# Kernel tuning notes

Hardware: AMD Instinct MI355X
Metric: run time of the kernel (lower is better)

Reference implementation:

```python
import jax, jax.numpy as jnp
import numpy as np
import math

D_MODEL = 1024
NUM_HEADS = 16
D_K = D_MODEL // NUM_HEADS
THETA = 10000.0
B, T = 2, 2048


def _trunc_normal(key, shape, std):
    # truncated normal in [-3std, 3std]
    return jax.random.truncated_normal(key, -3.0, 3.0, shape, jnp.float32) * std


def setup_inputs() -> dict:
    key = jax.random.key(0)
    ks = jax.random.split(key, 6)
    sigma = math.sqrt(2.0 / (D_MODEL + D_MODEL))
    x = jax.random.normal(ks[0], (B, T, D_MODEL), jnp.float32)
    Wq = _trunc_normal(ks[1], (D_MODEL, D_MODEL), sigma)  # [out, in]
    Wk = _trunc_normal(ks[2], (D_MODEL, D_MODEL), sigma)
    Wv = _trunc_normal(ks[3], (D_MODEL, D_MODEL), sigma)
    Wo = _trunc_normal(ks[4], (D_MODEL, D_MODEL), sigma)
    token_positions = jnp.arange(T, dtype=jnp.int64 if jax.config.read('jax_enable_x64') else jnp.int32)
    return {"x": x, "Wq": Wq, "Wk": Wk, "Wv": Wv, "Wo": Wo,
            "token_positions": token_positions}


def _rotate_half(x):
    x0 = x[..., ::2]
    x1 = x[..., 1::2]
    return jnp.stack((-x1, x0), axis=-1).reshape(x.shape)


def _rope(x, token_positions):
    # x: [B, H, T, d_k]; token_positions: [T]
    inv_freq = 1.0 / (THETA ** (jnp.arange(0, D_K, 2, dtype=jnp.float32) / D_K))
    ang = token_positions.astype(jnp.float32)[:, None] * inv_freq  # [T, d_k/2]
    cos = jnp.repeat(jnp.cos(ang), 2, axis=-1)  # [T, d_k]
    sin = jnp.repeat(jnp.sin(ang), 2, axis=-1)
    xdtype = x.dtype
    xf = x.astype(jnp.float32)
    return (xf * cos + _rotate_half(xf) * sin).astype(xdtype)


def reference(x, Wq, Wk, Wv, Wo, token_positions):
    b, t, _ = x.shape

    def proj_split(W):
        h = jnp.einsum('btd,od->bto', x, W)
        return h.reshape(b, t, NUM_HEADS, D_K).transpose(0, 2, 1, 3)  # [B,H,T,d_k]

    Q = _rope(proj_split(Wq), token_positions)
    K = _rope(proj_split(Wk), token_positions)
    V = proj_split(Wv)

    scores = jnp.einsum('bhqd,bhkd->bhqk', Q, K) / math.sqrt(D_K)
    causal = jnp.tril(jnp.ones((t, t), dtype=bool))  # [T,T]
    scores = jnp.where(causal, scores, -jnp.inf)
    weights = jax.nn.softmax(scores, axis=-1)
    attn = jnp.einsum('bhqk,bhkd->bhqd', weights, V)  # [B,H,T,d_v]
    merged = attn.transpose(0, 2, 1, 3).reshape(b, t, D_MODEL)
    return jnp.einsum('btd,od->bto', merged, Wo)
```

## Files before the change

### kernel.cpp

```cpp
#include <hip/hip_runtime.h>
#include <cstdint>
#include <cstddef>

#define DMODEL 1024
#define NHEADS 16
#define DKH    64
#define SEQT   2048
#define NBATCH 2
#define MTOT   (NBATCH*SEQT)

#define QSCALE 0.1803368801111204f

using h16   = _Float16;
using h16x2 = __attribute__((ext_vector_type(2))) h16;
using h16x4 = __attribute__((ext_vector_type(4))) h16;
using h16x8 = __attribute__((ext_vector_type(8))) h16;
using f32x4 = __attribute__((ext_vector_type(4))) float;
using fp16x2_native = __attribute__((ext_vector_type(2))) __fp16;

using as1_void = __attribute__((address_space(1))) void;
using as3_void = __attribute__((address_space(3))) void;

__device__ __forceinline__ void gll16(void* lds, const void* g) {
  __builtin_amdgcn_global_load_lds((const as1_void*)g, (as3_void*)lds, 16, 0, 0);
}

__device__ __forceinline__ h16x2 pkrtz(float a, float b) {
  fp16x2_native t = __builtin_amdgcn_cvt_pkrtz(a, b);
  h16x2 r; r[0] = (h16)t[0]; r[1] = (h16)t[1]; return r;
}

__device__ __forceinline__ h16x4 cvt4(const float4 v) {
  h16x4 o; o[0] = (h16)v.x; o[1] = (h16)v.y; o[2] = (h16)v.z; o[3] = (h16)v.w; return o;
}

__global__ void prep_kernel(const float4* __restrict__ x,
                            const float4* __restrict__ Wq, const float4* __restrict__ Wk,
                            const float4* __restrict__ Wv, const float4* __restrict__ Wo,
                            h16x4* __restrict__ xb,
                            h16x4* __restrict__ wqb, h16x4* __restrict__ wkb,
                            h16x4* __restrict__ wvb, h16x4* __restrict__ wob,
                            float* __restrict__ ctab, float* __restrict__ stab) {
  const int tid  = blockIdx.x * blockDim.x + threadIdx.x;
  const int nthr = gridDim.x * blockDim.x;
  const int NX4 = MTOT * DMODEL / 4;
  const int NW4 = DMODEL * DMODEL / 4;
  for (int i = tid; i < NX4; i += nthr) xb[i] = cvt4(x[i]);
  for (int i = tid; i < NW4; i += nthr) {
    wqb[i] = cvt4(Wq[i]);
    wkb[i] = cvt4(Wk[i]);
    wvb[i] = cvt4(Wv[i]);
    wob[i] = cvt4(Wo[i]);
  }
  for (int i = tid; i < SEQT * 32; i += nthr) {
    const int t = i >> 5, fi = i & 31;
    float inv = __expf(-0.28782313662425575f * (float)fi);
    float ang = (float)t * inv;
    float s, c;
    sincosf(ang, &s, &c);
    ctab[i] = c; stab[i] = s;
  }
}

__device__ __forceinline__ void gemm128_bt(const h16* __restrict__ A, const h16* __restrict__ Bt,
                                           int m0, int n0, h16* Al, h16* Bl, f32x4 acc[4][4]) {
  const int tid  = threadIdx.x;
  const int lane = tid & 63;
  const int wv   = tid >> 6;
  const int wm = (wv >> 1) * 64, wn = (wv & 1) * 64;
  const int lr = lane & 15, lk = (lane >> 4) * 8;
  const int srow = tid >> 2, scol = (tid & 3) * 8;
  const h16* a0 = A  + (size_t)(m0 + srow) * DMODEL + scol;
  const h16* a1 = a0 + (size_t)64 * DMODEL;
  const h16* b0 = Bt + (size_t)(n0 + srow) * DMODEL + scol;
  const h16* b1 = b0 + (size_t)64 * DMODEL;
  h16* alds0 = Al + wv * 512;
  h16* alds1 = Al + 2048 + wv * 512;
  h16* blds0 = Bl + wv * 512;
  h16* blds1 = Bl + 2048 + wv * 512;

  for (int k0 = 0; k0 < DMODEL; k0 += 32) {
    __syncthreads();
    gll16(alds0, a0 + k0);
    gll16(alds1, a1 + k0);
    gll16(blds0, b0 + k0);
    gll16(blds1, b1 + k0);
    __syncthreads();
    h16x8 af[4], bfr[4];
#pragma unroll
    for (int i = 0; i < 4; ++i) {
      af[i]  = *(const h16x8*)(Al + (wm + i * 16 + lr) * 32 + lk);
      bfr[i] = *(const h16x8*)(Bl + (wn + i * 16 + lr) * 32 + lk);
    }
#pragma unroll
    for (int i = 0; i < 4; ++i)
#pragma unroll
      for (int j = 0; j < 4; ++j)
        acc[i][j] = __builtin_amdgcn_mfma_f32_16x16x32_f16(af[i], bfr[j], acc[i][j], 0, 0, 0);
  }
}

__global__ __launch_bounds__(256, 2) void qkv_kernel(
    const h16* __restrict__ xb,
    const h16* __restrict__ wqb, const h16* __restrict__ wkb, const h16* __restrict__ wvb,
    const float* __restrict__ ctab, const float* __restrict__ stab,
    h16* __restrict__ Qb, h16* __restrict__ Kb, h16* __restrict__ Vt) {
  __shared__ h16 Al[128 * 32], Bl[128 * 32];
  const int which = blockIdx.z;
  const h16* W = (which == 0) ? wqb : (which == 1) ? wkb : wvb;
  const int m0 = blockIdx.x * 128, n0 = blockIdx.y * 128;
  f32x4 acc[4][4];
  const f32x4 zero4 = {0.f, 0.f, 0.f, 0.f};
#pragma unroll
  for (int i = 0; i < 4; ++i)
#pragma unroll
    for (int j = 0; j < 4; ++j) acc[i][j] = zero4;

  gemm128_bt(xb, W, m0, n0, Al, Bl, acc);

  const int lane = threadIdx.x & 63, wv = threadIdx.x >> 6;
  const int wm = (wv >> 1) * 64, wn = (wv & 1) * 64;
  const int lr4 = ((lane >> 4) << 2), lc = lane & 15;
  if (which == 2) {
#pragma unroll
    for (int i = 0; i < 4; ++i) {
      const int m = m0 + wm + i * 16 + lr4;
      const int b = m >> 11, t = m & (SEQT - 1);
#pragma unroll
      for (int j = 0; j < 4; ++j) {
        const int n = n0 + wn + j * 16 + lc;
        const int h = n >> 6, d = n & 63;
        h16x4 o4;
#pragma unroll
        for (int r = 0; r < 4; ++r) o4[r] = (h16)acc[i][j][r];
        *(h16x4*)&Vt[((size_t)(b * NHEADS + h) * DKH + d) * SEQT + t] = o4;
      }
    }
  } else {
#pragma unroll
    for (int i = 0; i < 4; ++i) {
#pragma unroll
      for (int j = 0; j < 4; ++j) {
        const int n = n0 + wn + j * 16 + lc;
        const int h = n >> 6, d = n & 63;
#pragma unroll
        for (int r = 0; r < 4; ++r) {
          const int m = m0 + wm + i * 16 + lr4 + r;
          const int b = m >> 11, t = m & (SEQT - 1);
          float v = acc[i][j][r];
          float pv = __shfl_xor(v, 1);
          const int fi = d >> 1;
          float c = ctab[t * 32 + fi], s = stab[t * 32 + fi];
          float res = (d & 1) ? (v * c + pv * s) : (v * c - pv * s);
          if (which == 0) res *= QSCALE;
          h16* dst = (which == 0) ? Qb : Kb;
          dst[((size_t)(b * NHEADS + h) * SEQT + t) * DKH + d] = (h16)res;
        }
      }
    }
  }
}

__global__ __launch_bounds__(256, 4) void attn_kernel(
    const h16* __restrict__ Qb, const h16* __restrict__ Kb,
    const h16* __restrict__ Vt, h16* __restrict__ Mg) {
  __shared__ h16 Kl[128][76];
  __shared__ h16 Vl[64][140];
  const int linear = blockIdx.x + 32 * blockIdx.y;
  const int v   = linear & 7;
  const int p   = linear >> 3;
  const int w   = p >> 5;
  const int c32 = p & 31;
  const int u   = (c32 + w) & 3;
  const int bh  = c32;
  const int qt  = (u == 0) ? v : (u == 1) ? (15 - v) : (u == 2) ? (16 + v) : (31 - v);
  const int b = bh >> 4, h = bh & 15;
  const int tid = threadIdx.x, lane = tid & 63, wv = tid >> 6;
  const int lr = lane & 15, lg = lane >> 4;
  const int q0 = qt * 64;
  const int qbase = q0 + wv * 16;
  const int q = qbase + lr;
  const h16* Qp = Qb + ((size_t)bh * SEQT + qbase) * DKH;
  const h16* Kp = Kb + (size_t)bh * SEQT * DKH;
  const h16* Vp = Vt + (size_t)bh * DKH * SEQT;

  h16x8 qf[2];
#pragma unroll
  for (int kk = 0; kk < 2; ++kk)
    qf[kk] = *(const h16x8*)(Qp + lr * DKH + kk * 32 + lg * 8);

  float mrow = -3.0e38f, lsum = 0.f;
  f32x4 o[4];
  const f32x4 zero4 = {0.f, 0.f, 0.f, 0.f};
#pragma unroll
  for (int di = 0; di < 4; ++di) o[di] = zero4;

  const int sr = tid >> 2, sc = (tid & 3) * 16;
  uint4 ka0, ka1, ka2, ka3;
  uint4 va0, va1, va2, va3;

#define KISSUE(k0_) {                                                      \
    const h16* kb_ = Kp + (size_t)(k0_) * DKH;                             \
    ka0 = *(const uint4*)(kb_ + (size_t)sr * DKH + sc);                    \
    ka1 = *(const uint4*)(kb_ + (size_t)sr * DKH + sc + 8);                \
    ka2 = *(const uint4*)(kb_ + (size_t)(64 + sr) * DKH + sc);             \
    ka3 = *(const uint4*)(kb_ + (size_t)(64 + sr) * DKH + sc + 8);         \
  }
#define KWRITE() {                                                         \
    *(uint4*)&Kl[sr][sc]          = ka0;                                   \
    *(uint4*)&Kl[sr][sc + 8]      = ka1;                                   \
    *(uint4*)&Kl[64 + sr][sc]     = ka2;                                   \
    *(uint4*)&Kl[64 + sr][sc + 8] = ka3;                                   \
  }
#define VISSUE(k0_) {                                                      \
    const h16* vb_ = Vp + (k0_);                                           \
    va0 = *(const uint4*)(vb_ + (size_t)sr * SEQT + sc);                   \
    va1 = *(const uint4*)(vb_ + (size_t)sr * SEQT + sc + 8);               \
    va2 = *(const uint4*)(vb_ + (size_t)sr * SEQT + 64 + sc);              \
    va3 = *(const uint4*)(vb_ + (size_t)sr * SEQT + 64 + sc + 8);          \
  }
#define VWRITE() {                                                         \
    *(uint4*)&Vl[sr][sc]          = va0;                                   \
    *(uint4*)&Vl[sr][sc + 8]      = va1;                                   \
    *(uint4*)&Vl[sr][64 + sc]     = va2;                                   \
    *(uint4*)&Vl[sr][64 + sc + 8] = va3;                                   \
  }

  KISSUE(0); VISSUE(0);
  KWRITE(); VWRITE();
  __syncthreads();

  const int nkt = (qt >> 1) + 1;
  for (int kt = 0; kt < nkt; ++kt) {
    const int k0 = kt * 128;
    const bool more = (kt + 1 < nkt);

    if (more) { KISSUE(k0 + 128); __builtin_amdgcn_sched_barrier(0); }

    f32x4 s[8];
    __builtin_amdgcn_s_setprio(1);
#pragma unroll
    for (int ni = 0; ni < 8; ++ni) {
      s[ni] = zero4;
#pragma unroll
      for (int kk = 0; kk < 2; ++kk) {
        h16x8 kf = *(const h16x8*)&Kl[ni * 16 + lr][kk * 32 + lg * 8];
        s[ni] = __builtin_amdgcn_mfma_f32_16x16x32_f16(kf, qf[kk], s[ni], 0, 0, 0);
      }
    }
    __builtin_amdgcn_s_setprio(0);

    __syncthreads();
    if (more) {
      KWRITE();
      VISSUE(k0 + 128); __builtin_amdgcn_sched_barrier(0);
    }

    if (kt == nkt - 1) {
#pragma unroll
      for (int ni = 0; ni < 8; ++ni)
#pragma unroll
        for (int r = 0; r < 4; ++r) {
          const int key = k0 + ni * 16 + lg * 4 + r;
          if (key > q) s[ni][r] = -3.0e38f;
        }
    }

    float mx = s[0][0];
#pragma unroll
    for (int ni = 0; ni < 8; ++ni)
#pragma unroll
      for (int r = 0; r < 4; ++r) mx = fmaxf(mx, s[ni][r]);
    mx = fmaxf(mx, __shfl_xor(mx, 16));
    mx = fmaxf(mx, __shfl_xor(mx, 32));
    if (mx > mrow + 11.0f) {
      const float mnew = fmaxf(mrow, mx);
      const float scl = exp2f(mrow - mnew);
      mrow = mnew;
      lsum *= scl;
#pragma unroll
      for (int di = 0; di < 4; ++di)
#pragma unroll
        for (int r = 0; r < 4; ++r) o[di][r] *= scl;
    }
    float rs = 0.f;
#pragma unroll
    for (int ni = 0; ni < 8; ++ni)
#pragma unroll
      for (int r = 0; r < 4; ++r) {
        float p2 = exp2f(s[ni][r] - mrow);
        s[ni][r] = p2;
        rs += p2;
      }
    rs += __shfl_xor(rs, 16);
    rs += __shfl_xor(rs, 32);
    lsum += rs;

    __builtin_amdgcn_s_setprio(1);
#pragma unroll
    for (int ni = 0; ni < 8; ++ni) {
      h16x2 plo = pkrtz(s[ni][0], s[ni][1]);
      h16x2 phi = pkrtz(s[ni][2], s[ni][3]);
      h16x4 pb; pb[0] = plo[0]; pb[1] = plo[1]; pb[2] = phi[0]; pb[3] = phi[1];
#pragma unroll
      for (int di = 0; di < 4; ++di) {
        h16x4 va = *(const h16x4*)&Vl[di * 16 + lr][ni * 16 + lg * 4];
        o[di] = __builtin_amdgcn_mfma_f32_16x16x16f16(va, pb, o[di], 0, 0, 0);
      }
    }
    __builtin_amdgcn_s_setprio(0);

    __syncthreads();
    if (more) VWRITE();
  }
#undef KISSUE
#undef KWRITE
#undef VISSUE
#undef VWRITE

  __syncthreads();
  const float inv = 1.0f / lsum;
#pragma unroll
  for (int di = 0; di < 4; ++di) {
    h16x2 lo = pkrtz(o[di][0] * inv, o[di][1] * inv);
    h16x2 hi = pkrtz(o[di][2] * inv, o[di][3] * inv);
    h16x4 o4; o4[0] = lo[0]; o4[1] = lo[1]; o4[2] = hi[0]; o4[3] = hi[1];
    *(h16x4*)&Kl[wv * 16 + lr][di * 16 + lg * 4] = o4;
  }
  __syncthreads();
  {
    const int row = tid >> 2, c0 = (tid & 3) * 16;
    h16* dst = Mg + ((size_t)(b * SEQT + q0 + row)) * DMODEL + h * DKH + c0;
    *(uint4*)dst       = *(const uint4*)&Kl[row][c0];
    *(uint4*)(dst + 8) = *(const uint4*)&Kl[row][c0 + 8];
  }
}

__global__ __launch_bounds__(256, 2) void proj_kernel(
    const h16* __restrict__ Mg, const h16* __restrict__ wob, float* __restrict__ out) {
  __shared__ h16 Al[128 * 32], Bl[128 * 32];
  const int m0 = blockIdx.x * 128, n0 = blockIdx.y * 128;
  f32x4 acc[4][4];
  const f32x4 zero4 = {0.f, 0.f, 0.f, 0.f};
#pragma unroll
  for (int i = 0; i < 4; ++i)
#pragma unroll
    for (int j = 0; j < 4; ++j) acc[i][j] = zero4;

  gemm128_bt(Mg, wob, m0, n0, Al, Bl, acc);

  const int lane = threadIdx.x & 63, wv = threadIdx.x >> 6;
  const int wm = (wv >> 1) * 64, wn = (wv & 1) * 64;
  const int lr4 = ((lane >> 4) << 2), lc = lane & 15;
#pragma unroll
  for (int i = 0; i < 4; ++i)
#pragma unroll
    for (int j = 0; j < 4; ++j) {
      const int n = n0 + wn + j * 16 + lc;
#pragma unroll
      for (int r = 0; r < 4; ++r) {
        const int m = m0 + wm + i * 16 + lr4 + r;
        out[(size_t)m * DMODEL + n] = acc[i][j][r];
      }
    }
}

extern "C" void kernel_launch(void* const* d_in, const int* in_sizes, int n_in,
                              void* d_out, int out_size, void* d_ws, size_t ws_size,
                              hipStream_t stream) {
  (void)in_sizes; (void)n_in; (void)out_size; (void)ws_size;
  const float* x  = (const float*)d_in[0];
  const float* Wq = (const float*)d_in[1];
  const float* Wk = (const float*)d_in[2];
  const float* Wv = (const float*)d_in[3];
  const float* Wo = (const float*)d_in[4];
  float* out = (float*)d_out;

  char* w = (char*)d_ws;
  h16* xb  = (h16*)w; w += (size_t)MTOT * DMODEL * 2;
  h16* wqb = (h16*)w; w += (size_t)DMODEL * DMODEL * 2;
  h16* wkb = (h16*)w; w += (size_t)DMODEL * DMODEL * 2;
  h16* wvb = (h16*)w; w += (size_t)DMODEL * DMODEL * 2;
  h16* wob = (h16*)w; w += (size_t)DMODEL * DMODEL * 2;
  h16* Qb  = (h16*)w; w += (size_t)MTOT * DMODEL * 2;
  h16* Kb  = (h16*)w; w += (size_t)MTOT * DMODEL * 2;
  h16* Vt  = (h16*)w; w += (size_t)MTOT * DMODEL * 2;
  h16* Mg  = (h16*)w; w += (size_t)MTOT * DMODEL * 2;
  float* ctab = (float*)w; w += (size_t)SEQT * 32 * 4;
  float* stab = (float*)w; w += (size_t)SEQT * 32 * 4;

  prep_kernel<<<1024, 256, 0, stream>>>((const float4*)x, (const float4*)Wq, (const float4*)Wk,
                                        (const float4*)Wv, (const float4*)Wo,
                                        (h16x4*)xb, (h16x4*)wqb, (h16x4*)wkb, (h16x4*)wvb,
                                        (h16x4*)wob, ctab, stab);
  qkv_kernel<<<dim3(32, 8, 3), 256, 0, stream>>>(xb, wqb, wkb, wvb, ctab, stab, Qb, Kb, Vt);
  attn_kernel<<<dim3(32, 32), 256, 0, stream>>>(Qb, Kb, Vt, Mg);
  proj_kernel<<<dim3(32, 8), 256, 0, stream>>>(Mg, wob, out);
}
```

Baseline: 117.5 us.

## Load V fragments directly from global memory instead of staging through LDS

Removes the shared-memory tile for V. Each lane now loads its MFMA operand fragments straight from global (or L2) memory into registers, double-buffered across the four output column blocks. This drops the LDS write/read traffic and frees LDS, which could raise occupancy. The cost is many small 8-byte uncoalesced global loads issued inside the loop, with latency that may be poorly hidden. The last __syncthreads stays in place.

```diff
diff --git a/kernel.cpp b/kernel.cpp
--- a/kernel.cpp
+++ b/kernel.cpp
@@ -165,7 +165,6 @@
     const h16* __restrict__ Qb, const h16* __restrict__ Kb,
     const h16* __restrict__ Vt, h16* __restrict__ Mg) {
   __shared__ h16 Kl[128][76];
-  __shared__ h16 Vl[64][140];
   const int linear = blockIdx.x + 32 * blockIdx.y;
   const int v   = linear & 7;
   const int p   = linear >> 3;
@@ -197,7 +196,6 @@
 
   const int sr = tid >> 2, sc = (tid & 3) * 16;
   uint4 ka0, ka1, ka2, ka3;
-  uint4 va0, va1, va2, va3;
 
 #define KISSUE(k0_) {                                                      \
     const h16* kb_ = Kp + (size_t)(k0_) * DKH;                             \
@@ -212,22 +210,9 @@
     *(uint4*)&Kl[64 + sr][sc]     = ka2;                                   \
     *(uint4*)&Kl[64 + sr][sc + 8] = ka3;                                   \
   }
-#define VISSUE(k0_) {                                                      \
-    const h16* vb_ = Vp + (k0_);                                           \
-    va0 = *(const uint4*)(vb_ + (size_t)sr * SEQT + sc);                   \
-    va1 = *(const uint4*)(vb_ + (size_t)sr * SEQT + sc + 8);               \
-    va2 = *(const uint4*)(vb_ + (size_t)sr * SEQT + 64 + sc);              \
-    va3 = *(const uint4*)(vb_ + (size_t)sr * SEQT + 64 + sc + 8);          \
-  }
-#define VWRITE() {                                                         \
-    *(uint4*)&Vl[sr][sc]          = va0;                                   \
-    *(uint4*)&Vl[sr][sc + 8]      = va1;                                   \
-    *(uint4*)&Vl[sr][64 + sc]     = va2;                                   \
-    *(uint4*)&Vl[sr][64 + sc + 8] = va3;                                   \
-  }
-
-  KISSUE(0); VISSUE(0);
-  KWRITE(); VWRITE();
+
+  KISSUE(0);
+  KWRITE();
   __syncthreads();
 
   const int nkt = (qt >> 1) + 1;
@@ -250,11 +235,16 @@
     }
     __builtin_amdgcn_s_setprio(0);
 
+    const h16* Vg = Vp + (size_t)lr * SEQT + k0 + lg * 4;
+    h16x4 vA[8], vB[8];
+#pragma unroll
+    for (int ni = 0; ni < 8; ++ni) vA[ni] = *(const h16x4*)(Vg + ni * 16);
+#pragma unroll
+    for (int ni = 0; ni < 8; ++ni) vB[ni] = *(const h16x4*)(Vg + 16 * SEQT + ni * 16);
+    __builtin_amdgcn_sched_barrier(0);
+
     __syncthreads();
-    if (more) {
-      KWRITE();
-      VISSUE(k0 + 128); __builtin_amdgcn_sched_barrier(0);
-    }
+    if (more) KWRITE();
 
     if (kt == nkt - 1) {
 #pragma unroll
@@ -296,27 +286,37 @@
     rs += __shfl_xor(rs, 32);
     lsum += rs;
 
-    __builtin_amdgcn_s_setprio(1);
+    h16x4 pb[8];
 #pragma unroll
     for (int ni = 0; ni < 8; ++ni) {
       h16x2 plo = pkrtz(s[ni][0], s[ni][1]);
       h16x2 phi = pkrtz(s[ni][2], s[ni][3]);
-      h16x4 pb; pb[0] = plo[0]; pb[1] = plo[1]; pb[2] = phi[0]; pb[3] = phi[1];
-#pragma unroll
-      for (int di = 0; di < 4; ++di) {
-        h16x4 va = *(const h16x4*)&Vl[di * 16 + lr][ni * 16 + lg * 4];
-        o[di] = __builtin_amdgcn_mfma_f32_16x16x16f16(va, pb, o[di], 0, 0, 0);
-      }
-    }
+      pb[ni][0] = plo[0]; pb[ni][1] = plo[1]; pb[ni][2] = phi[0]; pb[ni][3] = phi[1];
+    }
+
+    __builtin_amdgcn_s_setprio(1);
+#pragma unroll
+    for (int ni = 0; ni < 8; ++ni)
+      o[0] = __builtin_amdgcn_mfma_f32_16x16x16f16(vA[ni], pb[ni], o[0], 0, 0, 0);
+#pragma unroll
+    for (int ni = 0; ni < 8; ++ni) vA[ni] = *(const h16x4*)(Vg + 32 * SEQT + ni * 16);
+#pragma unroll
+    for (int ni = 0; ni < 8; ++ni)
+      o[1] = __builtin_amdgcn_mfma_f32_16x16x16f16(vB[ni], pb[ni], o[1], 0, 0, 0);
+#pragma unroll
+    for (int ni = 0; ni < 8; ++ni) vB[ni] = *(const h16x4*)(Vg + 48 * SEQT + ni * 16);
+#pragma unroll
+    for (int ni = 0; ni < 8; ++ni)
+      o[2] = __builtin_amdgcn_mfma_f32_16x16x16f16(vA[ni], pb[ni], o[2], 0, 0, 0);
+#pragma unroll
+    for (int ni = 0; ni < 8; ++ni)
+      o[3] = __builtin_amdgcn_mfma_f32_16x16x16f16(vB[ni], pb[ni], o[3], 0, 0, 0);
     __builtin_amdgcn_s_setprio(0);
 
     __syncthreads();
-    if (more) VWRITE();
   }
 #undef KISSUE
 #undef KWRITE
-#undef VISSUE
-#undef VWRITE
 
   __syncthreads();
   const float inv = 1.0f / lsum;
```

Measured after the change: 216.9 us. 1.85x slower.
